# Optimization experiments

Measured on AMD Instinct MI355X. Metric: run time of the kernel, lower is better.

The kernel has to match this reference:

```python
import jax, jax.numpy as jnp
import numpy as np

N_ITERS = 30  # fixed-iteration surrogate for the data-dependent while-loop power iteration
BN_EPS = 1e-5


def conv1x1(x, w, b):
    # x: [B,C,H,W], w: [O,C], b: [O]
    return jnp.einsum('bchw,oc->bohw', x, w) + b[None, :, None, None]


def bn_relu(x, gamma, beta):
    # training-mode BatchNorm2d (batch statistics over B,H,W per channel) + ReLU
    mean = jnp.mean(x, axis=(0, 2, 3), keepdims=True)
    var = jnp.var(x, axis=(0, 2, 3), keepdims=True)
    xn = (x - mean) * jax.lax.rsqrt(var + BN_EPS)
    return jax.nn.relu(gamma[None, :, None, None] * xn + beta[None, :, None, None])


def power_iteration_u(W, v0):
    # W: [B, N, M]  (N = H*W, M = mid_ch), v0: [B, M]
    # Batched power iteration on W^T W; returns leading left singular vector u: [B, N]
    Ws = jnp.einsum('bnm,bnk->bmk', W, W)  # [B, M, M]

    def step(v, _):
        v = jnp.einsum('bmk,bk->bm', Ws, v)
        v = v / jnp.linalg.norm(v, axis=-1, keepdims=True)
        return v, None

    v, _ = jax.lax.scan(step, v0, None, length=N_ITERS)
    u = jnp.einsum('bnm,bm->bn', W, v)
    u = u / jnp.linalg.norm(u, axis=-1, keepdims=True)
    return u


def setup_inputs() -> dict:
    key = jax.random.key(0)
    B, C, H, W = 32, 64, 128, 128
    M = C // 8  # mid_ch = in_ch // k
    ks = jax.random.split(key, 10)
    he = np.sqrt(2.0 / C).astype(np.float32)
    inp = {
        'x': jax.random.normal(ks[0], (B, C, H, W), dtype=jnp.float32),
        'f_w': jax.random.normal(ks[1], (M, C), dtype=jnp.float32) * he,
        'f_b': jnp.zeros((M,), jnp.float32),
        'f_gamma': jnp.ones((M,), jnp.float32),
        'f_beta': jnp.zeros((M,), jnp.float32),
        'g_w': jax.random.normal(ks[2], (M, C), dtype=jnp.float32) * he,
        'g_b': jnp.zeros((M,), jnp.float32),
        'g_gamma': jnp.ones((M,), jnp.float32),
        'g_beta': jnp.zeros((M,), jnp.float32),
        'h_w': jax.random.normal(ks[3], (M, C), dtype=jnp.float32) * he,
        'h_b': jnp.zeros((M,), jnp.float32),
        'v_w': jax.random.normal(ks[4], (C, M), dtype=jnp.float32) * np.sqrt(2.0 / M).astype(np.float32),
        'v_b': jnp.zeros((C,), jnp.float32),
        'v0f': jax.random.normal(ks[5], (B, M), dtype=jnp.float32),
        'v0g': jax.random.normal(ks[6], (B, M), dtype=jnp.float32),
    }
    return inp


def reference(x, f_w, f_b, f_gamma, f_beta, g_w, g_b, g_gamma, g_beta,
              h_w, h_b, v_w, v_b, v0f, v0g):
    B, C, H, W = x.shape
    M = f_w.shape[0]
    N = H * W
    # f, g: conv1x1 + BN + ReLU; h: conv1x1; all reshaped to [B, N, M]
    fx = bn_relu(conv1x1(x, f_w, f_b), f_gamma, f_beta).reshape(B, M, N).transpose(0, 2, 1)
    gx = bn_relu(conv1x1(x, g_w, g_b), g_gamma, g_beta).reshape(B, M, N).transpose(0, 2, 1)
    hx = conv1x1(x, h_w, h_b).reshape(B, M, N).transpose(0, 2, 1)
    # per-sample leading left singular vectors (batched power iteration)
    uf = power_iteration_u(fx, v0f)  # [B, N]
    ug = power_iteration_u(gx, v0g)  # [B, N]
    # z = u_f @ (u_g^T @ h_x)  -> rank-1 attention, [B, N, M]
    coef = jnp.einsum('bn,bnm->bm', ug, hx)       # [B, M]
    z = uf[:, :, None] * coef[:, None, :]         # [B, N, M]
    z = z.transpose(0, 2, 1).reshape(B, M, H, W)
    z = conv1x1(z, v_w, v_b)
    return z + x
```

## Files before the change

### kernel.cpp

```cpp
#include <hip/hip_runtime.h>

#define BB   32
#define CC   64
#define MM   8
#define NSP  16384
#define CNTF 524288.0f

typedef float f32x4 __attribute__((ext_vector_type(4)));
typedef unsigned int u32x2 __attribute__((ext_vector_type(2)));

#define OFF_FXP_B    0ull
#define OFF_GXP_B    8388608ull
#define OFF_HX_B     16777216ull
#define OFF_PSTATS_B 25165824ull
#define OFF_PWSA_B   (OFF_PSTATS_B + 512ull*32*4)
#define OFF_STATS_B  (OFF_PWSA_B + 32ull*3*4*64*4)

#define AXPY(A, WS, XV) \
    (A).x = fmaf((WS), (XV).x, (A).x); (A).y = fmaf((WS), (XV).y, (A).y); \
    (A).z = fmaf((WS), (XV).z, (A).z); (A).w = fmaf((WS), (XV).w, (A).w);

__device__ __forceinline__ unsigned pk_bf2(float a, float b) {
    unsigned ua = __float_as_uint(a); ua += 0x7FFFu + ((ua >> 16) & 1u);
    unsigned ub = __float_as_uint(b); ub += 0x7FFFu + ((ub >> 16) & 1u);
    return (ua >> 16) | (ub & 0xFFFF0000u);
}
__device__ __forceinline__ float lo16(unsigned u) { return __uint_as_float(u << 16); }
__device__ __forceinline__ float hi16(unsigned u) { return __uint_as_float(u & 0xFFFF0000u); }

__global__ __launch_bounds__(256, 2) void k_conv(const float* __restrict__ x,
        const float* __restrict__ fw, const float* __restrict__ gw,
        const float* __restrict__ hw,
        const float* __restrict__ fb, const float* __restrict__ gb,
        const float* __restrict__ hb, char* __restrict__ wsb) {
    __shared__ float wt[1536];
    __shared__ float sred[4][32];
    for (int i = threadIdx.x; i < 1536; i += 256) {
        int c = i / 24, k = i % 24;
        wt[i] = (k < 8) ? fw[k * 64 + c]
              : (k < 16) ? gw[(k - 8) * 64 + c]
                         : hw[(k - 16) * 64 + c];
    }
    __syncthreads();

    int g  = blockIdx.x * 256 + threadIdx.x;
    int b  = g >> 12;
    int n0 = (g & 4095) * 4;

    const float* xp = x + (size_t)b * CC * NSP + n0;

    float4 af[8], ag[8], ah[8];
#pragma unroll
    for (int m = 0; m < 8; ++m) {
        float bf = fb[m], bg = gb[m], bh = hb[m];
        af[m] = make_float4(bf, bf, bf, bf);
        ag[m] = make_float4(bg, bg, bg, bg);
        ah[m] = make_float4(bh, bh, bh, bh);
    }

#pragma unroll 8
    for (int c = 0; c < 64; ++c) {
        float4 xv = *(const float4*)(xp + (size_t)c * NSP);
        const float4* w4 = (const float4*)(&wt[c * 24]);
        float4 wf0 = w4[0], wf1 = w4[1], wg0 = w4[2], wg1 = w4[3], wh0 = w4[4], wh1 = w4[5];
        AXPY(af[0], wf0.x, xv); AXPY(af[1], wf0.y, xv); AXPY(af[2], wf0.z, xv); AXPY(af[3], wf0.w, xv);
        AXPY(af[4], wf1.x, xv); AXPY(af[5], wf1.y, xv); AXPY(af[6], wf1.z, xv); AXPY(af[7], wf1.w, xv);
        AXPY(ag[0], wg0.x, xv); AXPY(ag[1], wg0.y, xv); AXPY(ag[2], wg0.z, xv); AXPY(ag[3], wg0.w, xv);
        AXPY(ag[4], wg1.x, xv); AXPY(ag[5], wg1.y, xv); AXPY(ag[6], wg1.z, xv); AXPY(ag[7], wg1.w, xv);
        AXPY(ah[0], wh0.x, xv); AXPY(ah[1], wh0.y, xv); AXPY(ah[2], wh0.z, xv); AXPY(ah[3], wh0.w, xv);
        AXPY(ah[4], wh1.x, xv); AXPY(ah[5], wh1.y, xv); AXPY(ah[6], wh1.z, xv); AXPY(ah[7], wh1.w, xv);
    }

    unsigned short* fx16 = (unsigned short*)(wsb + OFF_FXP_B);
    unsigned short* gx16 = (unsigned short*)(wsb + OFF_GXP_B);
    unsigned short* hx16 = (unsigned short*)(wsb + OFF_HX_B);
    size_t base = (size_t)b * MM * NSP + n0;
#pragma unroll
    for (int m = 0; m < 8; ++m) {
        u32x2 pf; pf.x = pk_bf2(af[m].x, af[m].y); pf.y = pk_bf2(af[m].z, af[m].w);
        u32x2 pg; pg.x = pk_bf2(ag[m].x, ag[m].y); pg.y = pk_bf2(ag[m].z, ag[m].w);
        u32x2 ph; ph.x = pk_bf2(ah[m].x, ah[m].y); ph.y = pk_bf2(ah[m].z, ah[m].w);
        *(u32x2*)(fx16 + base + (size_t)m * NSP) = pf;
        *(u32x2*)(gx16 + base + (size_t)m * NSP) = pg;
        *(u32x2*)(hx16 + base + (size_t)m * NSP) = ph;
    }

    int wid = threadIdx.x >> 6, lane = threadIdx.x & 63;
#pragma unroll
    for (int m = 0; m < 8; ++m) {
        float fs = af[m].x + af[m].y + af[m].z + af[m].w;
        float fq = af[m].x * af[m].x + af[m].y * af[m].y + af[m].z * af[m].z + af[m].w * af[m].w;
        float gs = ag[m].x + ag[m].y + ag[m].z + ag[m].w;
        float gq = ag[m].x * ag[m].x + ag[m].y * ag[m].y + ag[m].z * ag[m].z + ag[m].w * ag[m].w;
#pragma unroll
        for (int o = 1; o < 64; o <<= 1) {
            fs += __shfl_xor(fs, o); fq += __shfl_xor(fq, o);
            gs += __shfl_xor(gs, o); gq += __shfl_xor(gq, o);
        }
        if (lane == 0) {
            sred[wid][m] = fs; sred[wid][8 + m] = fq;
            sred[wid][16 + m] = gs; sred[wid][24 + m] = gq;
        }
    }
    __syncthreads();
    if (threadIdx.x < 32) {
        float t = sred[0][threadIdx.x] + sred[1][threadIdx.x]
                + sred[2][threadIdx.x] + sred[3][threadIdx.x];
        ((float*)(wsb + OFF_PSTATS_B))[blockIdx.x * 32 + threadIdx.x] = t;
    }
}

__global__ __launch_bounds__(256) void k_gram(
        const float* __restrict__ fgam, const float* __restrict__ fbet,
        const float* __restrict__ ggam, const float* __restrict__ gbet,
        char* __restrict__ wsb) {
    int bid = blockIdx.x;
    int chunk = bid & 3, which = (bid >> 2) % 3, b = bid / 12;

    __shared__ float sst[8][32];
    __shared__ float stot[32];
    {
        int t32 = threadIdx.x & 31, seg = threadIdx.x >> 5;
        const float* ps = (const float*)(wsb + OFF_PSTATS_B);
        float s = 0.f;
#pragma unroll 8
        for (int i = 0; i < 64; ++i) s += ps[(seg * 64 + i) * 32 + t32];
        sst[seg][t32] = s;
    }
    __syncthreads();
    if (threadIdx.x < 32) {
        float t = 0.f;
#pragma unroll
        for (int w = 0; w < 8; ++w) t += sst[w][threadIdx.x];
        stot[threadIdx.x] = t;
        if (bid == 0) ((float*)(wsb + OFF_STATS_B))[threadIdx.x] = t;
    }
    __syncthreads();

    const float* st  = stot + (which == 0 ? 0 : 16);
    const float* gam = (which == 0) ? fgam : ggam;
    const float* bet = (which == 0) ? fbet : gbet;
    const float inv = 1.f / CNTF;
    float a[8], ccf[8];
#pragma unroll
    for (int m = 0; m < 8; ++m) {
        float mean = st[m] * inv;
        float var  = st[8 + m] * inv - mean * mean;
        float sc   = gam[m] / sqrtf(var + 1e-5f);
        a[m] = sc; ccf[m] = bet[m] - mean * sc;
    }

    const unsigned short* src = (const unsigned short*)
        (wsb + (which == 0 ? OFF_FXP_B : OFF_GXP_B)) + (size_t)b * MM * NSP;
    const unsigned short* hsrc = (const unsigned short*)
        (wsb + OFF_HX_B) + (size_t)b * MM * NSP;

    float acc[64];
#pragma unroll
    for (int j = 0; j < 64; ++j) acc[j] = 0.f;

#pragma unroll
    for (int i = 0; i < 4; ++i) {
        int n = (chunk * 1024 + i * 256 + threadIdx.x) * 4;
        float4 vv[8], hh[8];
#pragma unroll
        for (int m = 0; m < 8; ++m) {
            u32x2 u = *(const u32x2*)(src + (size_t)m * NSP + n);
            float4 t;
            t.x = fmaf(a[m], lo16(u.x), ccf[m]); t.x = t.x > 0.f ? t.x : 0.f;
            t.y = fmaf(a[m], hi16(u.x), ccf[m]); t.y = t.y > 0.f ? t.y : 0.f;
            t.z = fmaf(a[m], lo16(u.y), ccf[m]); t.z = t.z > 0.f ? t.z : 0.f;
            t.w = fmaf(a[m], hi16(u.y), ccf[m]); t.w = t.w > 0.f ? t.w : 0.f;
            vv[m] = t;
        }
        if (which == 2) {
#pragma unroll
            for (int m = 0; m < 8; ++m) {
                u32x2 u = *(const u32x2*)(hsrc + (size_t)m * NSP + n);
                hh[m] = make_float4(lo16(u.x), hi16(u.x), lo16(u.y), hi16(u.y));
            }
        } else {
#pragma unroll
            for (int m = 0; m < 8; ++m) hh[m] = vv[m];
        }
#pragma unroll
        for (int m2 = 0; m2 < 8; ++m2)
#pragma unroll
            for (int k = 0; k < 8; ++k) {
                float t = acc[m2 * 8 + k];
                t = fmaf(hh[m2].x, vv[k].x, t);
                t = fmaf(hh[m2].y, vv[k].y, t);
                t = fmaf(hh[m2].z, vv[k].z, t);
                t = fmaf(hh[m2].w, vv[k].w, t);
                acc[m2 * 8 + k] = t;
            }
    }

    int lane = threadIdx.x & 63;
#pragma unroll
    for (int s2 = 0; s2 < 6; ++s2) {
        int half = 32 >> s2;
        int up = (lane >> s2) & 1;
#pragma unroll
        for (int j = 0; j < 32; ++j) {
            if (j >= half) break;
            float send = up ? acc[j] : acc[j + half];
            float recv = __shfl_xor(send, 1 << s2);
            float keep = up ? acc[j + half] : acc[j];
            acc[j] = keep + recv;
        }
    }
    __shared__ float sacc[64];
    if (threadIdx.x < 64) sacc[threadIdx.x] = 0.f;
    __syncthreads();
    int rev = __brev((unsigned)lane) >> 26;
    atomicAdd(&sacc[rev], acc[0]);
    __syncthreads();
    float* pw = (float*)(wsb + OFF_PWSA_B) + (((size_t)b * 3 + which) * 4 + chunk) * 64;
    if (threadIdx.x < 64) pw[threadIdx.x] = sacc[threadIdx.x];
}

__global__ __launch_bounds__(256, 4) void k_out(const float* __restrict__ x,
        const float* __restrict__ fgam, const float* __restrict__ fbet,
        const float* __restrict__ vw, const float* __restrict__ vb,
        const float* __restrict__ v0f, const float* __restrict__ v0g,
        const char* __restrict__ wsb, float* __restrict__ out) {
    int bid = blockIdx.x;
    int b = bid >> 5, sub = bid & 31;
    int tile = sub & 15, ch0 = (sub >> 4) * 32;
    __shared__ float s_vfn[8], s_coef[8], s_w2[64];

    const float* pw = (const float*)(wsb + OFF_PWSA_B) + (size_t)b * 3 * 4 * 64;
    if (threadIdx.x < 16) {
        int grp = threadIdx.x >> 3, m = threadIdx.x & 7;
        float row[8];
#pragma unroll
        for (int k = 0; k < 8; ++k) {
            float s = 0.f;
#pragma unroll
            for (int ch = 0; ch < 4; ++ch) s += pw[(grp * 4 + ch) * 64 + m * 8 + k];
            row[k] = s;
        }
        float v = (grp == 0 ? v0f : v0g)[b * 8 + m];
        for (int it = 0; it < 30; ++it) {
            float t = 0.f;
#pragma unroll
            for (int k = 0; k < 8; ++k) t = fmaf(row[k], __shfl(v, k, 8), t);
            float s = t * t;
            s += __shfl_xor(s, 1, 8); s += __shfl_xor(s, 2, 8); s += __shfl_xor(s, 4, 8);
            v = t / sqrtf(s);
        }
        float t = 0.f;
#pragma unroll
        for (int k = 0; k < 8; ++k) t = fmaf(row[k], __shfl(v, k, 8), t);
        float s = v * t;
        s += __shfl_xor(s, 1, 8); s += __shfl_xor(s, 2, 8); s += __shfl_xor(s, 4, 8);
        float invn = 1.f / sqrtf(s);
        if (grp == 0) {
            s_vfn[m] = v * invn;
        } else {
            float cf = 0.f;
#pragma unroll
            for (int k = 0; k < 8; ++k) {
                float cr = 0.f;
#pragma unroll
                for (int ch = 0; ch < 4; ++ch) cr += pw[(2 * 4 + ch) * 64 + m * 8 + k];
                cf = fmaf(cr, __shfl(v, k, 8), cf);
            }
            s_coef[m] = cf * invn;
        }
    }
    __syncthreads();
    if (threadIdx.x < 64) {
        float acc = 0.f;
#pragma unroll
        for (int k = 0; k < 8; ++k) acc = fmaf(vw[threadIdx.x * 8 + k], s_coef[k], acc);
        s_w2[threadIdx.x] = acc;
    }
    __syncthreads();

    int n0 = tile * 1024 + threadIdx.x * 4;
    const float inv = 1.f / CNTF;
    const float* stats = (const float*)(wsb + OFF_STATS_B);
    const unsigned short* fx16 = (const unsigned short*)(wsb + OFF_FXP_B);

    float uf0 = 0.f, uf1 = 0.f, uf2 = 0.f, uf3 = 0.f;
#pragma unroll
    for (int m = 0; m < 8; ++m) {
        float mean = stats[m] * inv;
        float var  = stats[8 + m] * inv - mean * mean;
        float a    = fgam[m] / sqrtf(var + 1e-5f);
        float cc   = fbet[m] - mean * a;
        float vf   = s_vfn[m];
        u32x2 u = *(const u32x2*)(fx16 + (size_t)(b * 8 + m) * NSP + n0);
        float t0 = fmaf(a, lo16(u.x), cc); t0 = t0 > 0.f ? t0 : 0.f; uf0 = fmaf(vf, t0, uf0);
        float t1 = fmaf(a, hi16(u.x), cc); t1 = t1 > 0.f ? t1 : 0.f; uf1 = fmaf(vf, t1, uf1);
        float t2 = fmaf(a, lo16(u.y), cc); t2 = t2 > 0.f ? t2 : 0.f; uf2 = fmaf(vf, t2, uf2);
        float t3 = fmaf(a, hi16(u.y), cc); t3 = t3 > 0.f ? t3 : 0.f; uf3 = fmaf(vf, t3, uf3);
    }

    const float* xp = x   + (size_t)(b * CC + ch0) * NSP + n0;
    float*       op = out + (size_t)(b * CC + ch0) * NSP + n0;
#pragma unroll 8
    for (int c = 0; c < 32; ++c) {
        float w2c = s_w2[ch0 + c];
        float bc  = vb[ch0 + c];
        float4 xv = *(const float4*)(xp + (size_t)c * NSP);
        f32x4 ov;
        ov.x = fmaf(uf0, w2c, xv.x + bc);
        ov.y = fmaf(uf1, w2c, xv.y + bc);
        ov.z = fmaf(uf2, w2c, xv.z + bc);
        ov.w = fmaf(uf3, w2c, xv.w + bc);
        __builtin_nontemporal_store(ov, (f32x4*)(op + (size_t)c * NSP));
    }
}

extern "C" void kernel_launch(void* const* d_in, const int* in_sizes, int n_in,
                              void* d_out, int out_size, void* d_ws, size_t ws_size,
                              hipStream_t stream) {
    const float* x    = (const float*)d_in[0];
    const float* f_w  = (const float*)d_in[1];
    const float* f_b  = (const float*)d_in[2];
    const float* f_g  = (const float*)d_in[3];
    const float* f_be = (const float*)d_in[4];
    const float* g_w  = (const float*)d_in[5];
    const float* g_b  = (const float*)d_in[6];
    const float* g_g  = (const float*)d_in[7];
    const float* g_be = (const float*)d_in[8];
    const float* h_w  = (const float*)d_in[9];
    const float* h_b  = (const float*)d_in[10];
    const float* v_w  = (const float*)d_in[11];
    const float* v_b  = (const float*)d_in[12];
    const float* v0f  = (const float*)d_in[13];
    const float* v0g  = (const float*)d_in[14];
    char*  wsb = (char*)d_ws;
    float* out = (float*)d_out;

    k_conv<<<512,  256, 0, stream>>>(x, f_w, g_w, h_w, f_b, g_b, h_b, wsb);
    k_gram<<<384,  256, 0, stream>>>(f_g, f_be, g_g, g_be, wsb);
    k_out <<<1024, 256, 0, stream>>>(x, f_g, f_be, v_w, v_b, v0f, v0g, wsb, out);
}
```

Baseline: 115.5 us.

## Fuse conv and Gram kernels with a grid barrier, keeping activations in registers

Merges the conv1x1 and Gram-matrix kernels into one persistent kernel. A software grid-wide barrier over 512 blocks lets BatchNorm statistics be reduced globally, after which the Gram products are formed from register-resident f, g and h values. This removes writing and re-reading the bf16 g and h intermediates and one kernel launch. In exchange it adds a spin barrier that needs all 512 blocks co-resident, which could deadlock if occupancy falls short, plus a memset and more partial sums for k_out to reduce.

After: 246.0 us. 2.13x slower.

```diff
diff --git a/kernel.cpp b/kernel.cpp
--- a/kernel.cpp
+++ b/kernel.cpp
@@ -1,24 +1,20 @@
 #include <hip/hip_runtime.h>
 
-#define BB   32
-#define CC   64
-#define MM   8
-#define NSP  16384
-#define CNTF 524288.0f
+#define BB    32
+#define CC    64
+#define MM    8
+#define NSP   16384
+#define CNTF  524288.0f
+#define NBLK1 512
 
 typedef float f32x4 __attribute__((ext_vector_type(4)));
 typedef unsigned int u32x2 __attribute__((ext_vector_type(2)));
 
 #define OFF_FXP_B    0ull
-#define OFF_GXP_B    8388608ull
-#define OFF_HX_B     16777216ull
-#define OFF_PSTATS_B 25165824ull
+#define OFF_PSTATS_B 8388608ull
 #define OFF_PWSA_B   (OFF_PSTATS_B + 512ull*32*4)
-#define OFF_STATS_B  (OFF_PWSA_B + 32ull*3*4*64*4)
-
-#define AXPY(A, WS, XV) \
-    (A).x = fmaf((WS), (XV).x, (A).x); (A).y = fmaf((WS), (XV).y, (A).y); \
-    (A).z = fmaf((WS), (XV).z, (A).z); (A).w = fmaf((WS), (XV).w, (A).w);
+#define OFF_STATS_B  (OFF_PWSA_B + 512ull*192*4)
+#define OFF_BAR_B    (OFF_STATS_B + 32ull*4)
 
 __device__ __forceinline__ unsigned pk_bf2(float a, float b) {
     unsigned ua = __float_as_uint(a); ua += 0x7FFFu + ((ua >> 16) & 1u);
@@ -28,24 +24,68 @@
 __device__ __forceinline__ float lo16(unsigned u) { return __uint_as_float(u << 16); }
 __device__ __forceinline__ float hi16(unsigned u) { return __uint_as_float(u & 0xFFFF0000u); }
 
-__global__ __launch_bounds__(256, 2) void k_conv(const float* __restrict__ x,
+__device__ __forceinline__ float agent_loadf(const float* p) {
+    return __hip_atomic_load(p, __ATOMIC_RELAXED, __HIP_MEMORY_SCOPE_AGENT);
+}
+__device__ __forceinline__ void agent_storef(float* p, float v) {
+    __hip_atomic_store(p, v, __ATOMIC_RELAXED, __HIP_MEMORY_SCOPE_AGENT);
+}
+
+__device__ __forceinline__ void grid_barrier(int* cnt) {
+    __syncthreads();
+    if (threadIdx.x == 0) {
+        __threadfence();
+        __hip_atomic_fetch_add(cnt, 1, __ATOMIC_ACQ_REL, __HIP_MEMORY_SCOPE_AGENT);
+        while (__hip_atomic_load(cnt, __ATOMIC_ACQUIRE, __HIP_MEMORY_SCOPE_AGENT) < NBLK1)
+            __builtin_amdgcn_s_sleep(1);
+        __threadfence();
+    }
+    __syncthreads();
+}
+
+#define AXPY(A, WS, XV) \
+    (A).x = fmaf((WS), (XV).x, (A).x); (A).y = fmaf((WS), (XV).y, (A).y); \
+    (A).z = fmaf((WS), (XV).z, (A).z); (A).w = fmaf((WS), (XV).w, (A).w);
+
+#define BUTTERFLY32_ATOMIC(OFFSET) { \
+    _Pragma("unroll") for (int s2 = 0; s2 < 5; ++s2) { \
+        int half = 16 >> s2; int up = (lane >> s2) & 1; \
+        _Pragma("unroll") for (int j = 0; j < 16; ++j) { \
+            if (j >= half) break; \
+            float send = up ? acc[j] : acc[j + half]; \
+            float recv = __shfl_xor(send, 1 << s2); \
+            float keep = up ? acc[j + half] : acc[j]; \
+            acc[j] = keep + recv; } } \
+    float tot = acc[0] + __shfl_xor(acc[0], 32); \
+    if (lane < 32) atomicAdd(&sacc[(OFFSET) + (__brev((unsigned)lane) >> 27)], tot); }
+
+__global__ __launch_bounds__(256, 2) void k_fused1(const float* __restrict__ x,
         const float* __restrict__ fw, const float* __restrict__ gw,
         const float* __restrict__ hw,
         const float* __restrict__ fb, const float* __restrict__ gb,
-        const float* __restrict__ hb, char* __restrict__ wsb) {
+        const float* __restrict__ hb,
+        const float* __restrict__ fgam, const float* __restrict__ fbet,
+        const float* __restrict__ ggam, const float* __restrict__ gbet,
+        char* __restrict__ wsb) {
     __shared__ float wt[1536];
     __shared__ float sred[4][32];
+    __shared__ float sst[8][32];
+    __shared__ float stot[32];
+    __shared__ float sacc[192];
+
     for (int i = threadIdx.x; i < 1536; i += 256) {
         int c = i / 24, k = i % 24;
         wt[i] = (k < 8) ? fw[k * 64 + c]
               : (k < 16) ? gw[(k - 8) * 64 + c]
                          : hw[(k - 16) * 64 + c];
     }
+    if (threadIdx.x < 192) sacc[threadIdx.x] = 0.f;
     __syncthreads();
 
     int g  = blockIdx.x * 256 + threadIdx.x;
     int b  = g >> 12;
     int n0 = (g & 4095) * 4;
+    int wid = threadIdx.x >> 6, lane = threadIdx.x & 63;
 
     const float* xp = x + (size_t)b * CC * NSP + n0;
 
@@ -57,7 +97,6 @@
         ag[m] = make_float4(bg, bg, bg, bg);
         ah[m] = make_float4(bh, bh, bh, bh);
     }
-
 #pragma unroll 8
     for (int c = 0; c < 64; ++c) {
         float4 xv = *(const float4*)(xp + (size_t)c * NSP);
@@ -71,21 +110,16 @@
         AXPY(ah[4], wh1.x, xv); AXPY(ah[5], wh1.y, xv); AXPY(ah[6], wh1.z, xv); AXPY(ah[7], wh1.w, xv);
     }
 
-    unsigned short* fx16 = (unsigned short*)(wsb + OFF_FXP_B);
-    unsigned short* gx16 = (unsigned short*)(wsb + OFF_GXP_B);
-    unsigned short* hx16 = (unsigned short*)(wsb + OFF_HX_B);
-    size_t base = (size_t)b * MM * NSP + n0;
-#pragma unroll
-    for (int m = 0; m < 8; ++m) {
-        u32x2 pf; pf.x = pk_bf2(af[m].x, af[m].y); pf.y = pk_bf2(af[m].z, af[m].w);
-        u32x2 pg; pg.x = pk_bf2(ag[m].x, ag[m].y); pg.y = pk_bf2(ag[m].z, ag[m].w);
-        u32x2 ph; ph.x = pk_bf2(ah[m].x, ah[m].y); ph.y = pk_bf2(ah[m].z, ah[m].w);
-        *(u32x2*)(fx16 + base + (size_t)m * NSP) = pf;
-        *(u32x2*)(gx16 + base + (size_t)m * NSP) = pg;
-        *(u32x2*)(hx16 + base + (size_t)m * NSP) = ph;
-    }
-
-    int wid = threadIdx.x >> 6, lane = threadIdx.x & 63;
+    {
+        unsigned short* fx16 = (unsigned short*)(wsb + OFF_FXP_B);
+        size_t base = (size_t)b * MM * NSP + n0;
+#pragma unroll
+        for (int m = 0; m < 8; ++m) {
+            u32x2 pf; pf.x = pk_bf2(af[m].x, af[m].y); pf.y = pk_bf2(af[m].z, af[m].w);
+            *(u32x2*)(fx16 + base + (size_t)m * NSP) = pf;
+        }
+    }
+
 #pragma unroll
     for (int m = 0; m < 8; ++m) {
         float fs = af[m].x + af[m].y + af[m].z + af[m].w;
@@ -106,25 +140,17 @@
     if (threadIdx.x < 32) {
         float t = sred[0][threadIdx.x] + sred[1][threadIdx.x]
                 + sred[2][threadIdx.x] + sred[3][threadIdx.x];
-        ((float*)(wsb + OFF_PSTATS_B))[blockIdx.x * 32 + threadIdx.x] = t;
-    }
-}
-
-__global__ __launch_bounds__(256) void k_gram(
-        const float* __restrict__ fgam, const float* __restrict__ fbet,
-        const float* __restrict__ ggam, const float* __restrict__ gbet,
-        char* __restrict__ wsb) {
-    int bid = blockIdx.x;
-    int chunk = bid & 3, which = (bid >> 2) % 3, b = bid / 12;
-
-    __shared__ float sst[8][32];
-    __shared__ float stot[32];
+        agent_storef((float*)(wsb + OFF_PSTATS_B) + blockIdx.x * 32 + threadIdx.x, t);
+    }
+
+    grid_barrier((int*)(wsb + OFF_BAR_B));
+
     {
         int t32 = threadIdx.x & 31, seg = threadIdx.x >> 5;
         const float* ps = (const float*)(wsb + OFF_PSTATS_B);
         float s = 0.f;
 #pragma unroll 8
-        for (int i = 0; i < 64; ++i) s += ps[(seg * 64 + i) * 32 + t32];
+        for (int i = 0; i < 64; ++i) s += agent_loadf(ps + (seg * 64 + i) * 32 + t32);
         sst[seg][t32] = s;
     }
     __syncthreads();
@@ -133,91 +159,107 @@
 #pragma unroll
         for (int w = 0; w < 8; ++w) t += sst[w][threadIdx.x];
         stot[threadIdx.x] = t;
-        if (bid == 0) ((float*)(wsb + OFF_STATS_B))[threadIdx.x] = t;
-    }
-    __syncthreads();
-
-    const float* st  = stot + (which == 0 ? 0 : 16);
-    const float* gam = (which == 0) ? fgam : ggam;
-    const float* bet = (which == 0) ? fbet : gbet;
+        if (blockIdx.x == 0) ((float*)(wsb + OFF_STATS_B))[threadIdx.x] = t;
+    }
+    __syncthreads();
+
     const float inv = 1.f / CNTF;
-    float a[8], ccf[8];
-#pragma unroll
-    for (int m = 0; m < 8; ++m) {
-        float mean = st[m] * inv;
-        float var  = st[8 + m] * inv - mean * mean;
-        float sc   = gam[m] / sqrtf(var + 1e-5f);
-        a[m] = sc; ccf[m] = bet[m] - mean * sc;
-    }
-
-    const unsigned short* src = (const unsigned short*)
-        (wsb + (which == 0 ? OFF_FXP_B : OFF_GXP_B)) + (size_t)b * MM * NSP;
-    const unsigned short* hsrc = (const unsigned short*)
-        (wsb + OFF_HX_B) + (size_t)b * MM * NSP;
-
-    float acc[64];
-#pragma unroll
-    for (int j = 0; j < 64; ++j) acc[j] = 0.f;
-
-#pragma unroll
-    for (int i = 0; i < 4; ++i) {
-        int n = (chunk * 1024 + i * 256 + threadIdx.x) * 4;
-        float4 vv[8], hh[8];
-#pragma unroll
-        for (int m = 0; m < 8; ++m) {
-            u32x2 u = *(const u32x2*)(src + (size_t)m * NSP + n);
-            float4 t;
-            t.x = fmaf(a[m], lo16(u.x), ccf[m]); t.x = t.x > 0.f ? t.x : 0.f;
-            t.y = fmaf(a[m], hi16(u.x), ccf[m]); t.y = t.y > 0.f ? t.y : 0.f;
-            t.z = fmaf(a[m], lo16(u.y), ccf[m]); t.z = t.z > 0.f ? t.z : 0.f;
-            t.w = fmaf(a[m], hi16(u.y), ccf[m]); t.w = t.w > 0.f ? t.w : 0.f;
-            vv[m] = t;
-        }
-        if (which == 2) {
-#pragma unroll
-            for (int m = 0; m < 8; ++m) {
-                u32x2 u = *(const u32x2*)(hsrc + (size_t)m * NSP + n);
-                hh[m] = make_float4(lo16(u.x), hi16(u.x), lo16(u.y), hi16(u.y));
-            }
-        } else {
-#pragma unroll
-            for (int m = 0; m < 8; ++m) hh[m] = vv[m];
-        }
-#pragma unroll
-        for (int m2 = 0; m2 < 8; ++m2)
-#pragma unroll
-            for (int k = 0; k < 8; ++k) {
-                float t = acc[m2 * 8 + k];
-                t = fmaf(hh[m2].x, vv[k].x, t);
-                t = fmaf(hh[m2].y, vv[k].y, t);
-                t = fmaf(hh[m2].z, vv[k].z, t);
-                t = fmaf(hh[m2].w, vv[k].w, t);
-                acc[m2 * 8 + k] = t;
-            }
-    }
-
-    int lane = threadIdx.x & 63;
-#pragma unroll
-    for (int s2 = 0; s2 < 6; ++s2) {
-        int half = 32 >> s2;
-        int up = (lane >> s2) & 1;
-#pragma unroll
-        for (int j = 0; j < 32; ++j) {
-            if (j >= half) break;
-            float send = up ? acc[j] : acc[j + half];
-            float recv = __shfl_xor(send, 1 << s2);
-            float keep = up ? acc[j + half] : acc[j];
-            acc[j] = keep + recv;
-        }
-    }
-    __shared__ float sacc[64];
-    if (threadIdx.x < 64) sacc[threadIdx.x] = 0.f;
-    __syncthreads();
-    int rev = __brev((unsigned)lane) >> 26;
-    atomicAdd(&sacc[rev], acc[0]);
-    __syncthreads();
-    float* pw = (float*)(wsb + OFF_PWSA_B) + (((size_t)b * 3 + which) * 4 + chunk) * 64;
-    if (threadIdx.x < 64) pw[threadIdx.x] = sacc[threadIdx.x];
+
+    {
+        float scf[8], off_f[8];
+#pragma unroll
+        for (int m = 0; m < 8; ++m) {
+            float mean = stot[m] * inv;
+            float var  = stot[8 + m] * inv - mean * mean;
+            float s = fgam[m] / sqrtf(var + 1e-5f);
+            scf[m] = s; off_f[m] = fbet[m] - mean * s;
+        }
+        float fnx[8], fny[8], fnz[8], fnw[8];
+#pragma unroll
+        for (int m = 0; m < 8; ++m) {
+            float t;
+            t = fmaf(scf[m], af[m].x, off_f[m]); fnx[m] = t > 0.f ? t : 0.f;
+            t = fmaf(scf[m], af[m].y, off_f[m]); fny[m] = t > 0.f ? t : 0.f;
+            t = fmaf(scf[m], af[m].z, off_f[m]); fnz[m] = t > 0.f ? t : 0.f;
+            t = fmaf(scf[m], af[m].w, off_f[m]); fnw[m] = t > 0.f ? t : 0.f;
+        }
+#pragma unroll
+        for (int h2 = 0; h2 < 2; ++h2) {
+            float acc[32];
+#pragma unroll
+            for (int j = 0; j < 32; ++j) acc[j] = 0.f;
+#pragma unroll
+            for (int i = 0; i < 4; ++i)
+#pragma unroll
+                for (int j = 0; j < 8; ++j) {
+                    float t = acc[i * 8 + j];
+                    t = fmaf(fnx[h2 * 4 + i], fnx[j], t);
+                    t = fmaf(fny[h2 * 4 + i], fny[j], t);
+                    t = fmaf(fnz[h2 * 4 + i], fnz[j], t);
+                    t = fmaf(fnw[h2 * 4 + i], fnw[j], t);
+                    acc[i * 8 + j] = t;
+                }
+            BUTTERFLY32_ATOMIC(h2 * 32)
+        }
+    }
+    {
+        float scg[8], off_g[8];
+#pragma unroll
+        for (int m = 0; m < 8; ++m) {
+            float mean = stot[16 + m] * inv;
+            float var  = stot[24 + m] * inv - mean * mean;
+            float s = ggam[m] / sqrtf(var + 1e-5f);
+            scg[m] = s; off_g[m] = gbet[m] - mean * s;
+        }
+        float gnx[8], gny[8], gnz[8], gnw[8];
+#pragma unroll
+        for (int m = 0; m < 8; ++m) {
+            float t;
+            t = fmaf(scg[m], ag[m].x, off_g[m]); gnx[m] = t > 0.f ? t : 0.f;
+            t = fmaf(scg[m], ag[m].y, off_g[m]); gny[m] = t > 0.f ? t : 0.f;
+            t = fmaf(scg[m], ag[m].z, off_g[m]); gnz[m] = t > 0.f ? t : 0.f;
+            t = fmaf(scg[m], ag[m].w, off_g[m]); gnw[m] = t > 0.f ? t : 0.f;
+        }
+#pragma unroll
+        for (int h2 = 0; h2 < 2; ++h2) {
+            float acc[32];
+#pragma unroll
+            for (int j = 0; j < 32; ++j) acc[j] = 0.f;
+#pragma unroll
+            for (int i = 0; i < 4; ++i)
+#pragma unroll
+                for (int j = 0; j < 8; ++j) {
+                    float t = acc[i * 8 + j];
+                    t = fmaf(gnx[h2 * 4 + i], gnx[j], t);
+                    t = fmaf(gny[h2 * 4 + i], gny[j], t);
+                    t = fmaf(gnz[h2 * 4 + i], gnz[j], t);
+                    t = fmaf(gnw[h2 * 4 + i], gnw[j], t);
+                    acc[i * 8 + j] = t;
+                }
+            BUTTERFLY32_ATOMIC(64 + h2 * 32)
+        }
+#pragma unroll
+        for (int h2 = 0; h2 < 2; ++h2) {
+            float acc[32];
+#pragma unroll
+            for (int j = 0; j < 32; ++j) acc[j] = 0.f;
+#pragma unroll
+            for (int i = 0; i < 4; ++i)
+#pragma unroll
+                for (int j = 0; j < 8; ++j) {
+                    float t = acc[i * 8 + j];
+                    t = fmaf(ah[h2 * 4 + i].x, gnx[j], t);
+                    t = fmaf(ah[h2 * 4 + i].y, gny[j], t);
+                    t = fmaf(ah[h2 * 4 + i].z, gnz[j], t);
+                    t = fmaf(ah[h2 * 4 + i].w, gnw[j], t);
+                    acc[i * 8 + j] = t;
+                }
+            BUTTERFLY32_ATOMIC(128 + h2 * 32)
+        }
+    }
+    __syncthreads();
+    if (threadIdx.x < 192)
+        ((float*)(wsb + OFF_PWSA_B))[blockIdx.x * 192 + threadIdx.x] = sacc[threadIdx.x];
 }
 
 __global__ __launch_bounds__(256, 4) void k_out(const float* __restrict__ x,
@@ -230,7 +272,7 @@
     int tile = sub & 15, ch0 = (sub >> 4) * 32;
     __shared__ float s_vfn[8], s_coef[8], s_w2[64];
 
-    const float* pw = (const float*)(wsb + OFF_PWSA_B) + (size_t)b * 3 * 4 * 64;
+    const float* pw = (const float*)(wsb + OFF_PWSA_B) + (size_t)b * 16 * 192;
     if (threadIdx.x < 16) {
         int grp = threadIdx.x >> 3, m = threadIdx.x & 7;
         float row[8];
@@ -238,7 +280,7 @@
         for (int k = 0; k < 8; ++k) {
             float s = 0.f;
 #pragma unroll
-            for (int ch = 0; ch < 4; ++ch) s += pw[(grp * 4 + ch) * 64 + m * 8 + k];
+            for (int ch = 0; ch < 16; ++ch) s += pw[ch * 192 + grp * 64 + m * 8 + k];
             row[k] = s;
         }
         float v = (grp == 0 ? v0f : v0g)[b * 8 + m];
@@ -264,7 +306,7 @@
             for (int k = 0; k < 8; ++k) {
                 float cr = 0.f;
 #pragma unroll
-                for (int ch = 0; ch < 4; ++ch) cr += pw[(2 * 4 + ch) * 64 + m * 8 + k];
+                for (int ch = 0; ch < 16; ++ch) cr += pw[ch * 192 + 128 + m * 8 + k];
                 cf = fmaf(cr, __shfl(v, k, 8), cf);
             }
             s_coef[m] = cf * invn;
@@ -336,7 +378,9 @@
     char*  wsb = (char*)d_ws;
     float* out = (float*)d_out;
 
-    k_conv<<<512,  256, 0, stream>>>(x, f_w, g_w, h_w, f_b, g_b, h_b, wsb);
-    k_gram<<<384,  256, 0, stream>>>(f_g, f_be, g_g, g_be, wsb);
-    k_out <<<1024, 256, 0, stream>>>(x, f_g, f_be, v_w, v_b, v0f, v0g, wsb, out);
-}
+    (void)hipMemsetAsync(wsb + OFF_BAR_B, 0, 4, stream);
+
+    k_fused1<<<NBLK1, 256, 0, stream>>>(x, f_w, g_w, h_w, f_b, g_b, h_b,
+                                        f_g, f_be, g_g, g_be, wsb);
+    k_out  <<<1024,  256, 0, stream>>>(x, f_g, f_be, v_w, v_b, v0f, v0g, wsb, out);
+}
```
